# Kernel tuning notes

Measured on AMD Instinct MI355X. Metric: run time of the kernel, lower is better.

Reference implementation:

```python
import jax, jax.numpy as jnp
import numpy as np

N = 100_000      # nodes
E = 1_600_000    # edges (avg degree 16)
D_IN, D_HID, D_OUT = 128, 64, 64
NEG_SLOPE = 0.2  # PyG GATConv default


def setup_inputs() -> dict:
    key = jax.random.key(0)
    ks = jax.random.split(key, 10)
    s = lambda k, shape: jax.random.normal(k, shape, jnp.float32) * 0.1
    return {
        "x": jax.random.normal(ks[0], (N, D_IN), jnp.float32),
        "edge_index": jax.random.randint(ks[1], (2, E), 0, N, dtype=jnp.int32),
        "W1": s(ks[2], (D_IN, D_HID)),
        "a_src1": s(ks[3], (D_HID,)),
        "a_dst1": s(ks[4], (D_HID,)),
        "b1": jnp.zeros((D_HID,), jnp.float32),
        "W2": s(ks[5], (D_HID, D_OUT)),
        "a_src2": s(ks[6], (D_OUT,)),
        "a_dst2": s(ks[7], (D_OUT,)),
        "b2": jnp.zeros((D_OUT,), jnp.float32),
    }


def gat_conv(x, src, dst, W, a_src, a_dst, b):
    """Single-head PyG-style GATConv (self-loops already appended to src/dst)."""
    n = x.shape[0]
    h = x @ W                                   # [N, D]
    # per-edge attention logits: leaky_relu(a_src . h_j + a_dst . h_i)
    logit = jax.nn.leaky_relu((h @ a_src)[src] + (h @ a_dst)[dst], NEG_SLOPE)
    # segment softmax over incoming edges of each dst node
    m = jax.ops.segment_max(logit, dst, num_segments=n)
    e = jnp.exp(logit - m[dst])
    denom = jax.ops.segment_sum(e, dst, num_segments=n)
    alpha = e / (denom[dst] + 1e-16)            # [E]
    out = jax.ops.segment_sum(alpha[:, None] * h[src], dst, num_segments=n)
    return out + b


def reference(x, edge_index, W1, a_src1, a_dst1, b1, W2, a_src2, a_dst2, b2):
    n = x.shape[0]
    loops = jnp.arange(n, dtype=edge_index.dtype)  # add_self_loops=True default
    src = jnp.concatenate([edge_index[0], loops])
    dst = jnp.concatenate([edge_index[1], loops])
    h = gat_conv(x, src, dst, W1, a_src1, a_dst1, b1)
    embedding = jax.nn.relu(h)   # dropout = identity (inference semantics)
    out = gat_conv(embedding, src, dst, W2, a_src2, a_dst2, b2)
    return (embedding, out)
```

## Files before the change

### kernel.cpp

```cpp
#include <hip/hip_runtime.h>
#include <hip/hip_bf16.h>

#define DHID 64
#define SUBSH 9
#define SUBSZ (1 << SUBSH)
#define PCAP 16384
#define EB 2048
typedef __attribute__((ext_vector_type(8))) short short8;
typedef __attribute__((ext_vector_type(4))) float f32x4;

static __device__ __forceinline__ short tobf(float f) {
  __hip_bfloat16 h = __float2bfloat16(f);
  return *reinterpret_cast<short*>(&h);
}

__global__ __launch_bounds__(256)
void k_fusedA(const int* __restrict__ src, const int* __restrict__ dst,
              int* __restrict__ bkt, int* __restrict__ bcnt,
              int E, int nsb, int cap, int nbkt,
              const float* __restrict__ xf, const float* __restrict__ W1,
              const float* __restrict__ a_s, const float* __restrict__ a_d,
              short* __restrict__ hb, float* __restrict__ asb,
              float* __restrict__ adb, int N) {
  __shared__ int lcnt[256];
  __shared__ int lbase[256];
  __shared__ __align__(16) short ldsB[64 * 128];
  int tid = threadIdx.x;
  if (blockIdx.x < nbkt) {
    int c0 = blockIdx.x * EB;
    for (int i = tid; i < nsb; i += 256) lcnt[i] = 0;
    __syncthreads();
    int wloc[8], uloc[8], rloc[8];
    #pragma unroll
    for (int k = 0; k < 8; k++) {
      int i = c0 + tid + k * 256;
      if (i < E) {
        int d = dst[i];
        int w = d >> SUBSH;
        wloc[k] = w;
        uloc[k] = (src[i] << SUBSH) | (d & (SUBSZ - 1));
        rloc[k] = atomicAdd(&lcnt[w], 1);
      } else wloc[k] = -1;
    }
    __syncthreads();
    for (int i = tid; i < nsb; i += 256) lbase[i] = atomicAdd(&bcnt[i], lcnt[i]);
    __syncthreads();
    #pragma unroll
    for (int k = 0; k < 8; k++) {
      int w = wloc[k];
      if (w >= 0) bkt[(size_t)w * cap + lbase[w] + rloc[k]] = uloc[k];
    }
    return;
  }
  int n0 = (blockIdx.x - nbkt) * 64;
  for (int e = tid; e < 128 * 64; e += 256) {
    int k = e >> 6, c = e & 63;
    ldsB[c * 128 + (k ^ ((c & 7) << 3))] = tobf(W1[e]);
  }
  __syncthreads();

  int l = tid & 63, w = tid >> 6;
  int c = l & 15, g = l >> 4;
  f32x4 acc[4];
  #pragma unroll
  for (int t = 0; t < 4; t++) acc[t] = (f32x4){0.f, 0.f, 0.f, 0.f};

  int arow = 16 * w + c;
  int row0 = n0 + arow;
  const float* xr = xf + (size_t)row0 * 128;
  bool okr = row0 < N;
  short8 afr[4];
  #pragma unroll
  for (int s = 0; s < 4; s++) {
    int ke = s * 32 + g * 8;
    float4 u0 = make_float4(0.f, 0.f, 0.f, 0.f), u1 = u0;
    if (okr) { u0 = *(const float4*)(xr + ke); u1 = *(const float4*)(xr + ke + 4); }
    short8 af;
    af[0] = tobf(u0.x); af[1] = tobf(u0.y); af[2] = tobf(u0.z); af[3] = tobf(u0.w);
    af[4] = tobf(u1.x); af[5] = tobf(u1.y); af[6] = tobf(u1.z); af[7] = tobf(u1.w);
    afr[s] = af;
  }
  #pragma unroll
  for (int s = 0; s < 4; s++) {
    int ke = s * 32 + g * 8;
    #pragma unroll
    for (int t = 0; t < 4; t++) {
      int bcol = 16 * t + c;
      short8 bf = *(const short8*)(ldsB + bcol * 128 + (ke ^ ((bcol & 7) << 3)));
      acc[t] = __builtin_amdgcn_mfma_f32_16x16x32_bf16(afr[s], bf, acc[t], 0, 0, 0);
    }
  }
  float av_s[4], av_d[4];
  #pragma unroll
  for (int t = 0; t < 4; t++) { av_s[t] = a_s[16 * t + c]; av_d[t] = a_d[16 * t + c]; }
  #pragma unroll
  for (int q = 0; q < 4; q++) {
    int row = n0 + 16 * w + g * 4 + q;
    bool ok = row < N;
    float rs = 0.f, rd = 0.f;
    #pragma unroll
    for (int t = 0; t < 4; t++) {
      float v = acc[t][q];
      if (ok) hb[(size_t)row * 64 + 16 * t + c] = tobf(v);
      rs += v * av_s[t]; rd += v * av_d[t];
    }
    #pragma unroll
    for (int off = 1; off < 16; off <<= 1) {
      rs += __shfl_xor(rs, off, 64);
      rd += __shfl_xor(rd, off, 64);
    }
    if (ok && c == 0) { asb[row] = rs; adb[row] = rd; }
  }
}

__global__ __launch_bounds__(256)
void k_mgemm2(const short* __restrict__ eb, const float* __restrict__ W2,
              const float* __restrict__ a_s, const float* __restrict__ a_d,
              short* __restrict__ hb, float* __restrict__ asb,
              float* __restrict__ adb, int N) {
  __shared__ __align__(16) short lds[64 * 64 * 2];
  int tid = threadIdx.x;
  int n0 = blockIdx.x * 64;
  const char* ga = (const char*)eb + (size_t)n0 * 128;
  #pragma unroll
  for (int j = 0; j < 2; j++) {
    int d = j * 4096 + tid * 16;
    __builtin_amdgcn_global_load_lds(
        (__attribute__((address_space(1))) const void*)(ga + d),
        (__attribute__((address_space(3))) void*)((char*)lds + d), 16, 0, 0);
  }
  short* B = lds + 64 * 64;
  for (int e = tid; e < 64 * 64; e += 256) {
    int k = e >> 6, c = e & 63;
    B[c * 64 + (k ^ ((c & 7) << 3))] = tobf(W2[e]);
  }
  __syncthreads();

  int l = tid & 63, w = tid >> 6;
  int c = l & 15, g = l >> 4;
  const short* A = lds;
  f32x4 acc[4];
  #pragma unroll
  for (int t = 0; t < 4; t++) acc[t] = (f32x4){0.f, 0.f, 0.f, 0.f};
  int arow = 16 * w + c;
  #pragma unroll
  for (int s = 0; s < 2; s++) {
    int ke = s * 32 + g * 8;
    short8 af = *(const short8*)(A + arow * 64 + (ke ^ ((arow & 7) << 3)));
    #pragma unroll
    for (int t = 0; t < 4; t++) {
      int bcol = 16 * t + c;
      short8 bf = *(const short8*)(B + bcol * 64 + (ke ^ ((bcol & 7) << 3)));
      acc[t] = __builtin_amdgcn_mfma_f32_16x16x32_bf16(af, bf, acc[t], 0, 0, 0);
    }
  }
  float av_s[4], av_d[4];
  #pragma unroll
  for (int t = 0; t < 4; t++) { av_s[t] = a_s[16 * t + c]; av_d[t] = a_d[16 * t + c]; }
  #pragma unroll
  for (int q = 0; q < 4; q++) {
    int row = n0 + 16 * w + g * 4 + q;
    bool ok = row < N;
    float rs = 0.f, rd = 0.f;
    #pragma unroll
    for (int t = 0; t < 4; t++) {
      float v = acc[t][q];
      if (ok) hb[(size_t)row * 64 + 16 * t + c] = tobf(v);
      rs += v * av_s[t]; rd += v * av_d[t];
    }
    #pragma unroll
    for (int off = 1; off < 16; off <<= 1) {
      rs += __shfl_xor(rs, off, 64);
      rd += __shfl_xor(rd, off, 64);
    }
    if (ok && c == 0) { asb[row] = rs; adb[row] = rd; }
  }
}

__global__ void k_count(const int* __restrict__ bkt, const int* __restrict__ bcnt,
                        int* __restrict__ roff, int N, int cap) {
  __shared__ int h[SUBSZ];
  int sb = blockIdx.x, tid = threadIdx.x;
  for (int j = tid; j < SUBSZ; j += 256) h[j] = 1;
  __syncthreads();
  int n = bcnt[sb];
  const int* b = bkt + (size_t)sb * cap;
  for (int i = tid; i < n; i += 256) atomicAdd(&h[b[i] & (SUBSZ - 1)], 1);
  __syncthreads();
  int d0 = sb << SUBSH, d1 = min(N, d0 + SUBSZ);
  for (int j = tid; j < d1 - d0; j += 256) roff[d0 + j] = h[j];
}

__global__ void k_scan_block(int* __restrict__ buf, int n, int* __restrict__ bsum) {
  __shared__ int lds[256];
  int tid = threadIdx.x;
  int base = blockIdx.x * 1024 + tid * 4;
  int a0 = (base + 0) < n ? buf[base + 0] : 0;
  int a1 = (base + 1) < n ? buf[base + 1] : 0;
  int a2 = (base + 2) < n ? buf[base + 2] : 0;
  int a3 = (base + 3) < n ? buf[base + 3] : 0;
  int s = a0 + a1 + a2 + a3;
  lds[tid] = s; __syncthreads();
  for (int off = 1; off < 256; off <<= 1) {
    int t = (tid >= off) ? lds[tid - off] : 0;
    __syncthreads();
    lds[tid] += t;
    __syncthreads();
  }
  int excl = lds[tid] - s;
  if ((base + 0) < n) buf[base + 0] = excl; excl += a0;
  if ((base + 1) < n) buf[base + 1] = excl; excl += a1;
  if ((base + 2) < n) buf[base + 2] = excl; excl += a2;
  if ((base + 3) < n) buf[base + 3] = excl;
  if (tid == 255) bsum[blockIdx.x] = lds[255];
}

__global__ void k_scan_mid(int* __restrict__ bsum, int nb) {
  int lane = threadIdx.x;
  int v0 = (lane < nb) ? bsum[lane] : 0;
  #pragma unroll
  for (int off = 1; off < 64; off <<= 1) { int t = __shfl_up(v0, off, 64); if (lane >= off) v0 += t; }
  int v1 = (64 + lane) < nb ? bsum[64 + lane] : 0;
  #pragma unroll
  for (int off = 1; off < 64; off <<= 1) { int t = __shfl_up(v1, off, 64); if (lane >= off) v1 += t; }
  v1 += __shfl(v0, 63, 64);
  if (lane < nb) bsum[lane] = v0;
  if ((64 + lane) < nb) bsum[64 + lane] = v1;
}

__global__ void k_scan_add(int* __restrict__ buf, int n, const int* __restrict__ bsum, int nb) {
  int i = blockIdx.x * blockDim.x + threadIdx.x;
  if (i < n) { int c = i >> 10; if (c > 0) buf[i] += bsum[c - 1]; }
  if (i == 0) buf[n] = bsum[nb - 1];
}

__global__ void k_place(const int* __restrict__ bkt, const int* __restrict__ bcnt,
                        const int* __restrict__ roff, int* __restrict__ csr,
                        int N, int cap) {
  __shared__ int roff_l[SUBSZ + 1];
  __shared__ int lcnt[SUBSZ];
  __shared__ int stage[PCAP];
  int sb = blockIdx.x, tid = threadIdx.x;
  int d0 = sb << SUBSH;
  int d1 = min(N, d0 + SUBSZ);
  int nn = d1 - d0;
  for (int j = tid; j <= nn; j += 256) roff_l[j] = roff[d0 + j];
  for (int j = tid; j < SUBSZ; j += 256) lcnt[j] = 0;
  __syncthreads();
  int base = roff_l[0];
  int span = roff_l[nn] - base;
  int nE = bcnt[sb];
  const int* b = bkt + (size_t)sb * cap;
  if (span <= PCAP) {
    for (int d = tid; d < nn; d += 256) stage[roff_l[d] - base] = (d0 + d) << 7;
    for (int i = tid; i < nE; i += 256) {
      int u = b[i];
      int dl = u & (SUBSZ - 1);
      int rk = 1 + atomicAdd(&lcnt[dl], 1);
      stage[roff_l[dl] - base + rk] = (u >> SUBSH) << 7;
    }
    __syncthreads();
    for (int j = tid; j < span; j += 256) csr[base + j] = stage[j];
  } else {
    for (int d = tid; d < nn; d += 256) csr[roff_l[d]] = (d0 + d) << 7;
    for (int i = tid; i < nE; i += 256) {
      int u = b[i];
      int dl = u & (SUBSZ - 1);
      int rk = 1 + atomicAdd(&lcnt[dl], 1);
      csr[roff_l[dl] + rk] = (u >> SUBSH) << 7;
    }
  }
}

__global__ void k_agg(const int* __restrict__ roff, const int* __restrict__ csr,
                      const float* __restrict__ asb, const float* __restrict__ adb,
                      const short* __restrict__ hb, const float* __restrict__ b,
                      float* __restrict__ out, short* __restrict__ outb,
                      int N, int relu) {
  const char* hbase = (const char*)hb;
  int lane = threadIdx.x & 63;
  int colb = (lane & 15) * 8;
  int L = lane & 15;
  int wid = blockIdx.x * (blockDim.x >> 6) + (threadIdx.x >> 6);
  int nw = gridDim.x * (blockDim.x >> 6);
  float4 bv4 = ((const float4*)b)[L];
  for (int n = wid; n < N; n += nw) {
    int r0 = roff[n], r1 = roff[n + 1];
    float adn = adb[n];
    float a0 = 0.f, a1 = 0.f, a2 = 0.f, a3 = 0.f, denl = 0.f;
    for (int base = r0; base < r1; base += 64) {
      int cnt = min(64, r1 - base);
      int s128 = 0; float e = 0.f;
      if (lane < cnt) {
        s128 = csr[base + lane];
        float l = asb[s128 >> 7] + adn;
        l = fmaxf(l, 0.2f * l);
        e = __expf(l);
      }
      denl += e;
      int cntUp = (cnt + 3) & ~3;
      int addrv = (lane >> 4) << 2;
      #pragma unroll 4
      for (int j = 0; j < cntUp; j += 4) {
        int sofs = __builtin_amdgcn_ds_bpermute(addrv, s128);
        int ewi  = __builtin_amdgcn_ds_bpermute(addrv, (int)__float_as_uint(e));
        addrv += 16;
        float ew = __uint_as_float((unsigned)ewi);
        uint2 u = *(const uint2*)(hbase + (unsigned)(sofs + colb));
        a0 = fmaf(__uint_as_float(u.x << 16), ew, a0);
        a1 = fmaf(__uint_as_float(u.x & 0xFFFF0000u), ew, a1);
        a2 = fmaf(__uint_as_float(u.y << 16), ew, a2);
        a3 = fmaf(__uint_as_float(u.y & 0xFFFF0000u), ew, a3);
      }
    }
    #pragma unroll
    for (int off = 16; off <= 32; off <<= 1) {
      a0 += __shfl_xor(a0, off, 64); a1 += __shfl_xor(a1, off, 64);
      a2 += __shfl_xor(a2, off, 64); a3 += __shfl_xor(a3, off, 64);
    }
    float den = denl;
    #pragma unroll
    for (int off = 32; off; off >>= 1) den += __shfl_xor(den, off, 64);
    float inv = 1.f / (den + 1e-16f);
    if (lane < 16) {
      float4 o;
      o.x = fmaf(a0, inv, bv4.x); o.y = fmaf(a1, inv, bv4.y);
      o.z = fmaf(a2, inv, bv4.z); o.w = fmaf(a3, inv, bv4.w);
      if (relu) {
        o.x = fmaxf(o.x, 0.f); o.y = fmaxf(o.y, 0.f);
        o.z = fmaxf(o.z, 0.f); o.w = fmaxf(o.w, 0.f);
      }
      ((float4*)(out + (size_t)n * DHID))[L] = o;
      if (outb) {
        short4 ob = make_short4(tobf(o.x), tobf(o.y), tobf(o.z), tobf(o.w));
        ((short4*)(outb + (size_t)n * DHID))[L ^ ((n & 7) << 1)] = ob;
      }
    }
  }
}

extern "C" void kernel_launch(void* const* d_in, const int* in_sizes, int n_in,
                              void* d_out, int out_size, void* d_ws, size_t ws_size,
                              hipStream_t stream) {
  const float* x   = (const float*)d_in[0];
  const int*   ei  = (const int*)d_in[1];
  const float* W1  = (const float*)d_in[2];
  const float* as1 = (const float*)d_in[3];
  const float* ad1 = (const float*)d_in[4];
  const float* b1  = (const float*)d_in[5];
  const float* W2  = (const float*)d_in[6];
  const float* as2 = (const float*)d_in[7];
  const float* ad2 = (const float*)d_in[8];
  const float* b2  = (const float*)d_in[9];

  int N = in_sizes[0] / 128;
  int E = in_sizes[1] / 2;
  const int* srcp = ei;
  const int* dstp = ei + E;

  float* emb  = (float*)d_out;
  float* out2 = emb + (size_t)N * DHID;

  char* w = (char*)d_ws;
  auto alloc = [&](size_t bytes) { char* p = w; w += (bytes + 255) & ~(size_t)255; return p; };
  int NR = ((N + 63) / 64) * 64;
  int* roff = (int*)alloc((size_t)(N + 1) * 4);
  int* csr  = (int*)alloc((size_t)(E + N) * 4);
  int* bsum = (int*)alloc(2048);
  int* bcnt = (int*)alloc(1024);
  char* scr0 = alloc((size_t)NR * 128 * 2);
  short* hb = (short*)alloc((size_t)NR * 64 * 2);
  float* asb = (float*)alloc((size_t)N * 4);
  float* adb = (float*)alloc((size_t)N * 4);
  short* eb = (short*)scr0;
  int* bkt  = (int*)scr0;

  int nsb = (N + SUBSZ - 1) >> SUBSH;
  int cap = E / nsb + 4096;

  int nb = (N + 1023) / 1024;
  int NBLK = (N + 63) / 64;
  int nbkt = (E + EB - 1) / EB;

  hipMemsetAsync(bcnt, 0, (size_t)nsb * 4, stream);
  k_fusedA<<<nbkt + NBLK, 256, 0, stream>>>(srcp, dstp, bkt, bcnt, E, nsb, cap, nbkt,
                                            x, W1, as1, ad1, hb, asb, adb, N);
  k_count<<<nsb, 256, 0, stream>>>(bkt, bcnt, roff, N, cap);
  k_scan_block<<<nb, 256, 0, stream>>>(roff, N, bsum);
  k_scan_mid<<<1, 64, 0, stream>>>(bsum, nb);
  k_scan_add<<<(N + 255) / 256, 256, 0, stream>>>(roff, N, bsum, nb);
  k_place<<<nsb, 256, 0, stream>>>(bkt, bcnt, roff, csr, N, cap);

  k_agg<<<2048, 256, 0, stream>>>(roff, csr, asb, adb, hb, b1, emb, eb, N, 1);
  k_mgemm2<<<NBLK, 256, 0, stream>>>(eb, W2, as2, ad2, hb, asb, adb, N);
  k_agg<<<2048, 256, 0, stream>>>(roff, csr, asb, adb, hb, b2, out2, (short*)nullptr, N, 0);
}
```

Measured before the change: 180.5 us.

## Fuse CSR count, scan and placement into one kernel per sub-bucket

Replaces the count, three-stage scan and place kernels with a single kernel. Each block redundantly scans the per-bucket totals (bcnt plus self-loops) to get its global base offset, builds its local degree histogram, scans it in LDS and then places edges. This removes four launches and the global round trips for roff and bsum, at the cost of a redundant small scan in every block and a dependence on nsb fitting in 256. It also raises the unroll factor of the aggregation inner loop from 4 to 8.

```diff
diff --git a/kernel.cpp b/kernel.cpp
--- a/kernel.cpp
+++ b/kernel.cpp
@@ -114,6 +114,76 @@
 }
 
 __global__ __launch_bounds__(256)
+void k_place2(const int* __restrict__ bkt, const int* __restrict__ bcnt,
+              int* __restrict__ roff, int* __restrict__ csr,
+              int N, int nsb, int cap) {
+  __shared__ int scanbuf[256];
+  __shared__ int h[SUBSZ];
+  __shared__ int roff_l[SUBSZ + 1];
+  __shared__ int lcnt[SUBSZ];
+  __shared__ int stage[PCAP];
+  __shared__ int sbase;
+  int sb = blockIdx.x, tid = threadIdx.x;
+  int d0 = sb << SUBSH;
+  int nn = min(N - d0, SUBSZ);
+
+  int tot = 0;
+  if (tid < nsb) tot = bcnt[tid] + min(N - (tid << SUBSH), SUBSZ);
+  scanbuf[tid] = tot; __syncthreads();
+  for (int off = 1; off < 256; off <<= 1) {
+    int t = (tid >= off) ? scanbuf[tid - off] : 0;
+    __syncthreads(); scanbuf[tid] += t; __syncthreads();
+  }
+  if (tid == sb) sbase = scanbuf[tid] - tot;
+  __syncthreads();
+
+  for (int j = tid; j < SUBSZ; j += 256) { h[j] = 1; lcnt[j] = 0; }
+  __syncthreads();
+  int nE = bcnt[sb];
+  const int* b = bkt + (size_t)sb * cap;
+  for (int i = tid; i < nE; i += 256) atomicAdd(&h[b[i] & (SUBSZ - 1)], 1);
+  __syncthreads();
+
+  int a0 = h[2 * tid], a1 = h[2 * tid + 1];
+  int s = a0 + a1;
+  scanbuf[tid] = s; __syncthreads();
+  for (int off = 1; off < 256; off <<= 1) {
+    int t = (tid >= off) ? scanbuf[tid - off] : 0;
+    __syncthreads(); scanbuf[tid] += t; __syncthreads();
+  }
+  int excl = sbase + scanbuf[tid] - s;
+  roff_l[2 * tid] = excl;
+  roff_l[2 * tid + 1] = excl + a0;
+  if (tid == 255) roff_l[SUBSZ] = sbase + scanbuf[255];
+  __syncthreads();
+
+  for (int j = tid; j < nn; j += 256) roff[d0 + j] = roff_l[j];
+  if (d0 + nn == N && tid == 0) roff[N] = roff_l[nn];
+
+  int base0 = roff_l[0];
+  int span = roff_l[nn] - base0;
+  if (span <= PCAP) {
+    for (int d = tid; d < nn; d += 256) stage[roff_l[d] - base0] = (d0 + d) << 7;
+    for (int i = tid; i < nE; i += 256) {
+      int u = b[i];
+      int dl = u & (SUBSZ - 1);
+      int rk = 1 + atomicAdd(&lcnt[dl], 1);
+      stage[roff_l[dl] - base0 + rk] = (u >> SUBSH) << 7;
+    }
+    __syncthreads();
+    for (int j = tid; j < span; j += 256) csr[base0 + j] = stage[j];
+  } else {
+    for (int d = tid; d < nn; d += 256) csr[roff_l[d]] = (d0 + d) << 7;
+    for (int i = tid; i < nE; i += 256) {
+      int u = b[i];
+      int dl = u & (SUBSZ - 1);
+      int rk = 1 + atomicAdd(&lcnt[dl], 1);
+      csr[roff_l[dl] + rk] = (u >> SUBSH) << 7;
+    }
+  }
+}
+
+__global__ __launch_bounds__(256)
 void k_mgemm2(const short* __restrict__ eb, const float* __restrict__ W2,
               const float* __restrict__ a_s, const float* __restrict__ a_d,
               short* __restrict__ hb, float* __restrict__ asb,
@@ -174,101 +244,6 @@
       rd += __shfl_xor(rd, off, 64);
     }
     if (ok && c == 0) { asb[row] = rs; adb[row] = rd; }
-  }
-}
-
-__global__ void k_count(const int* __restrict__ bkt, const int* __restrict__ bcnt,
-                        int* __restrict__ roff, int N, int cap) {
-  __shared__ int h[SUBSZ];
-  int sb = blockIdx.x, tid = threadIdx.x;
-  for (int j = tid; j < SUBSZ; j += 256) h[j] = 1;
-  __syncthreads();
-  int n = bcnt[sb];
-  const int* b = bkt + (size_t)sb * cap;
-  for (int i = tid; i < n; i += 256) atomicAdd(&h[b[i] & (SUBSZ - 1)], 1);
-  __syncthreads();
-  int d0 = sb << SUBSH, d1 = min(N, d0 + SUBSZ);
-  for (int j = tid; j < d1 - d0; j += 256) roff[d0 + j] = h[j];
-}
-
-__global__ void k_scan_block(int* __restrict__ buf, int n, int* __restrict__ bsum) {
-  __shared__ int lds[256];
-  int tid = threadIdx.x;
-  int base = blockIdx.x * 1024 + tid * 4;
-  int a0 = (base + 0) < n ? buf[base + 0] : 0;
-  int a1 = (base + 1) < n ? buf[base + 1] : 0;
-  int a2 = (base + 2) < n ? buf[base + 2] : 0;
-  int a3 = (base + 3) < n ? buf[base + 3] : 0;
-  int s = a0 + a1 + a2 + a3;
-  lds[tid] = s; __syncthreads();
-  for (int off = 1; off < 256; off <<= 1) {
-    int t = (tid >= off) ? lds[tid - off] : 0;
-    __syncthreads();
-    lds[tid] += t;
-    __syncthreads();
-  }
-  int excl = lds[tid] - s;
-  if ((base + 0) < n) buf[base + 0] = excl; excl += a0;
-  if ((base + 1) < n) buf[base + 1] = excl; excl += a1;
-  if ((base + 2) < n) buf[base + 2] = excl; excl += a2;
-  if ((base + 3) < n) buf[base + 3] = excl;
-  if (tid == 255) bsum[blockIdx.x] = lds[255];
-}
-
-__global__ void k_scan_mid(int* __restrict__ bsum, int nb) {
-  int lane = threadIdx.x;
-  int v0 = (lane < nb) ? bsum[lane] : 0;
-  #pragma unroll
-  for (int off = 1; off < 64; off <<= 1) { int t = __shfl_up(v0, off, 64); if (lane >= off) v0 += t; }
-  int v1 = (64 + lane) < nb ? bsum[64 + lane] : 0;
-  #pragma unroll
-  for (int off = 1; off < 64; off <<= 1) { int t = __shfl_up(v1, off, 64); if (lane >= off) v1 += t; }
-  v1 += __shfl(v0, 63, 64);
-  if (lane < nb) bsum[lane] = v0;
-  if ((64 + lane) < nb) bsum[64 + lane] = v1;
-}
-
-__global__ void k_scan_add(int* __restrict__ buf, int n, const int* __restrict__ bsum, int nb) {
-  int i = blockIdx.x * blockDim.x + threadIdx.x;
-  if (i < n) { int c = i >> 10; if (c > 0) buf[i] += bsum[c - 1]; }
-  if (i == 0) buf[n] = bsum[nb - 1];
-}
-
-__global__ void k_place(const int* __restrict__ bkt, const int* __restrict__ bcnt,
-                        const int* __restrict__ roff, int* __restrict__ csr,
-                        int N, int cap) {
-  __shared__ int roff_l[SUBSZ + 1];
-  __shared__ int lcnt[SUBSZ];
-  __shared__ int stage[PCAP];
-  int sb = blockIdx.x, tid = threadIdx.x;
-  int d0 = sb << SUBSH;
-  int d1 = min(N, d0 + SUBSZ);
-  int nn = d1 - d0;
-  for (int j = tid; j <= nn; j += 256) roff_l[j] = roff[d0 + j];
-  for (int j = tid; j < SUBSZ; j += 256) lcnt[j] = 0;
-  __syncthreads();
-  int base = roff_l[0];
-  int span = roff_l[nn] - base;
-  int nE = bcnt[sb];
-  const int* b = bkt + (size_t)sb * cap;
-  if (span <= PCAP) {
-    for (int d = tid; d < nn; d += 256) stage[roff_l[d] - base] = (d0 + d) << 7;
-    for (int i = tid; i < nE; i += 256) {
-      int u = b[i];
-      int dl = u & (SUBSZ - 1);
-      int rk = 1 + atomicAdd(&lcnt[dl], 1);
-      stage[roff_l[dl] - base + rk] = (u >> SUBSH) << 7;
-    }
-    __syncthreads();
-    for (int j = tid; j < span; j += 256) csr[base + j] = stage[j];
-  } else {
-    for (int d = tid; d < nn; d += 256) csr[roff_l[d]] = (d0 + d) << 7;
-    for (int i = tid; i < nE; i += 256) {
-      int u = b[i];
-      int dl = u & (SUBSZ - 1);
-      int rk = 1 + atomicAdd(&lcnt[dl], 1);
-      csr[roff_l[dl] + rk] = (u >> SUBSH) << 7;
-    }
   }
 }
 
@@ -300,7 +275,7 @@
       denl += e;
       int cntUp = (cnt + 3) & ~3;
       int addrv = (lane >> 4) << 2;
-      #pragma unroll 4
+      #pragma unroll 8
       for (int j = 0; j < cntUp; j += 4) {
         int sofs = __builtin_amdgcn_ds_bpermute(addrv, s128);
         int ewi  = __builtin_amdgcn_ds_bpermute(addrv, (int)__float_as_uint(e));
@@ -366,7 +341,6 @@
   int NR = ((N + 63) / 64) * 64;
   int* roff = (int*)alloc((size_t)(N + 1) * 4);
   int* csr  = (int*)alloc((size_t)(E + N) * 4);
-  int* bsum = (int*)alloc(2048);
   int* bcnt = (int*)alloc(1024);
   char* scr0 = alloc((size_t)NR * 128 * 2);
   short* hb = (short*)alloc((size_t)NR * 64 * 2);
@@ -378,18 +352,13 @@
   int nsb = (N + SUBSZ - 1) >> SUBSH;
   int cap = E / nsb + 4096;
 
-  int nb = (N + 1023) / 1024;
   int NBLK = (N + 63) / 64;
   int nbkt = (E + EB - 1) / EB;
 
   hipMemsetAsync(bcnt, 0, (size_t)nsb * 4, stream);
   k_fusedA<<<nbkt + NBLK, 256, 0, stream>>>(srcp, dstp, bkt, bcnt, E, nsb, cap, nbkt,
                                             x, W1, as1, ad1, hb, asb, adb, N);
-  k_count<<<nsb, 256, 0, stream>>>(bkt, bcnt, roff, N, cap);
-  k_scan_block<<<nb, 256, 0, stream>>>(roff, N, bsum);
-  k_scan_mid<<<1, 64, 0, stream>>>(bsum, nb);
-  k_scan_add<<<(N + 255) / 256, 256, 0, stream>>>(roff, N, bsum, nb);
-  k_place<<<nsb, 256, 0, stream>>>(bkt, bcnt, roff, csr, N, cap);
+  k_place2<<<nsb, 256, 0, stream>>>(bkt, bcnt, roff, csr, N, nsb, cap);
 
   k_agg<<<2048, 256, 0, stream>>>(roff, csr, asb, adb, hb, b1, emb, eb, N, 1);
   k_mgemm2<<<NBLK, 256, 0, stream>>>(eb, W2, as2, ad2, hb, asb, adb, N);
```

New measurement: 173.8 us. 3.7% less time.
